# Kernel tuning notes

Hardware: AMD Instinct MI355X
Metric: run time of the kernel (lower is better)

The kernel has to match this reference:

```python
import jax, jax.numpy as jnp
import numpy as np

N = 50000      # nodes
E = 800000     # edges (avg degree 16)
G = 50         # graphs in batch (1000 nodes each)
D_IN, H, H2, OUT = 8, 128, 64, 1


def setup_inputs() -> dict:
    key = jax.random.key(0)
    ks = jax.random.split(key, 16)
    src = jax.random.randint(ks[0], (E,), 0, N)
    # every node gets at least one in-edge (forward computes 3/in_deg)
    dst = jnp.concatenate([jnp.arange(N), jax.random.randint(ks[1], (E - N,), 0, N)])
    graph_ids = jnp.arange(N) // (N // G)

    def lin(k, fan_in, fan_out):
        return jax.random.normal(k, (fan_in, fan_out), jnp.float32) / np.float32(np.sqrt(fan_in))

    inp = {"src": src, "dst": dst, "graph_ids": graph_ids}
    dims = [(D_IN, H), (H, H), (H, H), (H, H), (H, H)]
    for i, (fi, fo) in enumerate(dims):
        inp[f"W{i+1}"] = lin(ks[2 + i], fi, fo)
        inp[f"b{i+1}"] = jnp.zeros((fo,), jnp.float32)
    inp["lw1"] = lin(ks[8], H, H2)
    inp["lb1"] = jnp.zeros((H2,), jnp.float32)
    inp["lw2"] = lin(ks[9], H2, OUT)
    inp["lb2"] = jnp.zeros((OUT,), jnp.float32)
    return inp


def reference(src, dst, graph_ids, W1, b1, W2, b2, W3, b3, W4, b4, W5, b5, lw1, lb1, lw2, lb2):
    ones_e = jnp.ones((E,), jnp.float32)
    in_deg = jax.ops.segment_sum(ones_e, dst, num_segments=N)   # [N]
    out_deg = jax.ops.segment_sum(ones_e, src, num_segments=N)  # [N]

    # degree features (8 channels)
    h1 = in_deg[:, None]
    h2 = (in_deg > 3.0).astype(jnp.float32)[:, None]
    h3 = 3.0 / h1
    h4 = (in_deg > 4.0).astype(jnp.float32)[:, None]
    h_ = jnp.concatenate([h1, h2, h3, h4, -h1, -h2, -h3, -h4], axis=1)  # [N,8]

    # DGL GraphConv norm='both': clamp degrees to min 1 for normalization
    norm_src = jnp.maximum(out_deg, 1.0) ** -0.5  # [N]
    norm_dst = jnp.maximum(in_deg, 1.0) ** -0.5   # [N]

    def conv(h, W, b):
        m = (h * norm_src[:, None])[src]                        # [E, d] gather
        agg = jax.ops.segment_sum(m, dst, num_segments=N)       # [N, d] scatter-add
        return agg * norm_dst[:, None] @ W + b

    h_co = jax.nn.relu(conv(h_, W1, b1))
    h_co = jax.nn.relu(conv(h_co, W2, b2))
    h_co = jax.nn.relu(conv(h_co, W3, b3))
    h_co = jax.nn.relu(conv(h_co, W4, b4))
    h_co = jax.nn.relu(conv(h_co, W5, b5))                      # [N, H]

    # dgl.mean_nodes: per-graph mean pool
    counts = jax.ops.segment_sum(jnp.ones((N,), jnp.float32), graph_ids, num_segments=G)
    graph_emb = jax.ops.segment_sum(h_co, graph_ids, num_segments=G) / counts[:, None]  # [G, H]

    # dropout layers are identity in eval mode
    h_emb = jax.nn.relu(graph_emb @ lw1 + lb1)
    pred = jax.nn.sigmoid(h_emb @ lw2 + lb2)                    # [G, 1]
    return (pred, graph_emb, h_co)
```

## Files before the change

kernel.cpp:

```cpp
#include <hip/hip_runtime.h>
#include <math.h>

#define N_NODES 50000
#define N_EDGES 800000
#define N_GRAPHS 50
#define HD 128
#define TM 64
#define POOL_CHUNK 125
#define SCAN_B 256
#define SCAN_NB ((N_NODES + SCAN_B - 1) / SCAN_B)
#define NB_H 128
#define CH_H (N_EDGES / NB_H)
#define NBIN2 (N_NODES / 2)
#define ALDA 129

__global__ __launch_bounds__(256) void k_hist(const int* __restrict__ src,
                                              const int* __restrict__ dst,
                                              unsigned* __restrict__ part_in,
                                              unsigned* __restrict__ part_out) {
    __shared__ unsigned cnt[NBIN2];
    int t = threadIdx.x, b = blockIdx.x;
    int e0 = b * CH_H;
    for (int j = t; j < NBIN2; j += 256) cnt[j] = 0;
    __syncthreads();
    for (int e = e0 + t; e < e0 + CH_H; e += 256) {
        int i = dst[e];
        atomicAdd(&cnt[i >> 1], 1u << ((i & 1) * 16));
    }
    __syncthreads();
    for (int j = t; j < NBIN2; j += 256) part_in[b * NBIN2 + j] = cnt[j];
    __syncthreads();
    for (int j = t; j < NBIN2; j += 256) cnt[j] = 0;
    __syncthreads();
    for (int e = e0 + t; e < e0 + CH_H; e += 256) {
        int i = src[e];
        atomicAdd(&cnt[i >> 1], 1u << ((i & 1) * 16));
    }
    __syncthreads();
    for (int j = t; j < NBIN2; j += 256) part_out[b * NBIN2 + j] = cnt[j];
}

__global__ void k_dreduce(unsigned* __restrict__ part_in,
                          const unsigned* __restrict__ part_out,
                          int* __restrict__ deg_in, int* __restrict__ deg_out) {
    int j = blockIdx.x * blockDim.x + threadIdx.x;
    if (j >= NBIN2) return;
    unsigned run_i = 0, run_o = 0;
    for (int b = 0; b < NB_H; ++b) {
        unsigned pi = part_in[b * NBIN2 + j];
        unsigned po = part_out[b * NBIN2 + j];
        part_in[b * NBIN2 + j] = run_i;
        run_i += pi;
        run_o += po;
    }
    ((int2*)deg_in)[j] = make_int2((int)(run_i & 0xFFFFu), (int)(run_i >> 16));
    ((int2*)deg_out)[j] = make_int2((int)(run_o & 0xFFFFu), (int)(run_o >> 16));
}

__global__ void k_norms(const int* __restrict__ deg_in, const int* __restrict__ deg_out,
                        const int* __restrict__ gids,
                        float* norm_src, float* norm_dst, int* gcount,
                        float4* __restrict__ feat4) {
    __shared__ int hist[N_GRAPHS];
    int t = threadIdx.x;
    if (t < N_GRAPHS) hist[t] = 0;
    __syncthreads();
    int i = blockIdx.x * blockDim.x + t;
    if (i < N_NODES) {
        float di = (float)deg_in[i];
        float dq = (float)deg_out[i];
        float nd = 1.0f / sqrtf(fmaxf(di, 1.0f));
        float ns = 1.0f / sqrtf(fmaxf(dq, 1.0f));
        norm_dst[i] = nd;
        norm_src[i] = ns;
        float4 f;
        f.x = di * ns;
        f.y = (di > 3.0f) ? ns : 0.0f;
        f.z = (3.0f / di) * ns;
        f.w = (di > 4.0f) ? ns : 0.0f;
        feat4[i] = f;
        atomicAdd(&hist[gids[i]], 1);
    }
    __syncthreads();
    if (t < N_GRAPHS && hist[t] != 0) atomicAdd(&gcount[t], hist[t]);
}

__global__ void k_scan1(const int* __restrict__ deg_in, int* off, int* bsum) {
    __shared__ int sh[SCAN_B];
    int t = threadIdx.x;
    int i = blockIdx.x * SCAN_B + t;
    int v = (i < N_NODES) ? deg_in[i] : 0;
    sh[t] = v;
    __syncthreads();
    for (int o = 1; o < SCAN_B; o <<= 1) {
        int u = (t >= o) ? sh[t - o] : 0;
        __syncthreads();
        sh[t] += u;
        __syncthreads();
    }
    if (i < N_NODES) off[i] = sh[t] - v;
    if (t == SCAN_B - 1) bsum[blockIdx.x] = sh[t];
}

__global__ void k_scan2(int* bsum, int* off) {
    __shared__ int sh[SCAN_B];
    int t = threadIdx.x;
    int v = (t < SCAN_NB) ? bsum[t] : 0;
    sh[t] = v;
    __syncthreads();
    for (int o = 1; o < SCAN_B; o <<= 1) {
        int u = (t >= o) ? sh[t - o] : 0;
        __syncthreads();
        sh[t] += u;
        __syncthreads();
    }
    if (t < SCAN_NB) bsum[t] = sh[t] - v;
    if (t == SCAN_B - 1) off[N_NODES] = sh[t];
}

__global__ void k_scan3(int* off, const int* __restrict__ bsum) {
    int b = blockIdx.x, t = threadIdx.x;
    int i = b * SCAN_B + t;
    if (i < N_NODES) off[i] += bsum[b];
}

__global__ __launch_bounds__(256) void k_scatter2(const int* __restrict__ src,
                                                  const int* __restrict__ dst,
                                                  const int* __restrict__ off,
                                                  const unsigned* __restrict__ part_in,
                                                  int* __restrict__ csr) {
    __shared__ unsigned cur[NBIN2];
    int t = threadIdx.x, b = blockIdx.x;
    const unsigned* base = part_in + (size_t)b * NBIN2;
    for (int j = t; j < NBIN2; j += 256) cur[j] = base[j];
    __syncthreads();
    int e0 = b * CH_H;
    for (int e = e0 + t; e < e0 + CH_H; e += 256) {
        int d = dst[e];
        int sh = (d & 1) * 16;
        unsigned old = atomicAdd(&cur[d >> 1], 1u << sh);
        int rank = (int)((old >> sh) & 0xFFFFu);
        csr[off[d] + rank] = src[e];
    }
}

__global__ void k_agg1(const int* __restrict__ off, const int* __restrict__ csr,
                       const float4* __restrict__ feat4,
                       const float* __restrict__ ndst, float* __restrict__ agg8) {
    int i = blockIdx.x * blockDim.x + threadIdx.x;
    if (i >= N_NODES) return;
    int e0 = off[i], e1 = off[i + 1];
    float a0 = 0.f, a1 = 0.f, a2 = 0.f, a3 = 0.f;
    int e = e0;
    for (; e + 1 < e1; e += 2) {
        float4 f0 = feat4[csr[e]];
        float4 f1 = feat4[csr[e + 1]];
        a0 += f0.x + f1.x; a1 += f0.y + f1.y;
        a2 += f0.z + f1.z; a3 += f0.w + f1.w;
    }
    if (e < e1) {
        float4 f0 = feat4[csr[e]];
        a0 += f0.x; a1 += f0.y; a2 += f0.z; a3 += f0.w;
    }
    float nd = ndst[i];
    a0 *= nd; a1 *= nd; a2 *= nd; a3 *= nd;
    float4* p = (float4*)(agg8 + (size_t)i * 8);
    float4 hi = { a0, a1, a2, a3 };
    float4 lo = { -a0, -a1, -a2, -a3 };
    p[0] = hi;
    p[1] = lo;
}

__global__ void k_gemm1(const float* __restrict__ agg8, const float* __restrict__ W,
                        const float* __restrict__ b, const float* __restrict__ nsrc,
                        float* __restrict__ out) {
    __shared__ float Wsh[8 * 128];
    int t = threadIdx.x;
    for (int i = t; i < 1024; i += 256) Wsh[i] = W[i];
    __syncthreads();
    int row = blockIdx.x * 2 + (t >> 7);
    int j = t & 127;
    if (row >= N_NODES) return;
    const float* a = agg8 + (size_t)row * 8;
    float acc = b[j];
#pragma unroll
    for (int k = 0; k < 8; ++k) acc += a[k] * Wsh[k * 128 + j];
    out[(size_t)row * HD + j] = fmaxf(acc, 0.0f) * nsrc[row];
}

__global__ __launch_bounds__(256) void k_agg4(const int* __restrict__ off,
                                              const int* __restrict__ csr,
                                              const float* __restrict__ ndst,
                                              const float* __restrict__ h,
                                              float* __restrict__ out) {
    int wid = (blockIdx.x * blockDim.x + threadIdx.x) >> 6;
    int lane = threadIdx.x & 63;
    if (wid >= N_NODES) return;
    int half = lane >> 5;
    int q = lane & 31;
    int e0 = off[wid], e1 = off[wid + 1];
    float4 a = { 0.f, 0.f, 0.f, 0.f };
    int e = e0 + half;
    for (; e + 6 < e1; e += 8) {
        int s0 = csr[e], s1 = csr[e + 2], s2 = csr[e + 4], s3 = csr[e + 6];
        float4 v0 = *(const float4*)(h + (size_t)s0 * HD + q * 4);
        float4 v1 = *(const float4*)(h + (size_t)s1 * HD + q * 4);
        float4 v2 = *(const float4*)(h + (size_t)s2 * HD + q * 4);
        float4 v3 = *(const float4*)(h + (size_t)s3 * HD + q * 4);
        a.x += v0.x + v1.x + v2.x + v3.x;
        a.y += v0.y + v1.y + v2.y + v3.y;
        a.z += v0.z + v1.z + v2.z + v3.z;
        a.w += v0.w + v1.w + v2.w + v3.w;
    }
    for (; e < e1; e += 2) {
        int s0 = csr[e];
        float4 v0 = *(const float4*)(h + (size_t)s0 * HD + q * 4);
        a.x += v0.x; a.y += v0.y; a.z += v0.z; a.w += v0.w;
    }
    a.x += __shfl_xor(a.x, 32);
    a.y += __shfl_xor(a.y, 32);
    a.z += __shfl_xor(a.z, 32);
    a.w += __shfl_xor(a.w, 32);
    if (half == 0) {
        float nd = ndst[wid];
        a.x *= nd; a.y *= nd; a.z *= nd; a.w *= nd;
        *(float4*)(out + (size_t)wid * HD + q * 4) = a;
    }
}

__global__ void k_agg2(const int* __restrict__ off, const int* __restrict__ csr,
                       const float* __restrict__ ndst,
                       const float* __restrict__ h, float* __restrict__ out) {
    int wid = (blockIdx.x * blockDim.x + threadIdx.x) >> 6;
    int lane = threadIdx.x & 63;
    if (wid >= N_NODES) return;
    int e0 = off[wid], e1 = off[wid + 1];
    float a0 = 0.f, a1 = 0.f;
    int e = e0;
    for (; e + 3 < e1; e += 4) {
        int s0 = csr[e], s1 = csr[e + 1], s2 = csr[e + 2], s3 = csr[e + 3];
        float2 v0 = *(const float2*)(h + (size_t)s0 * HD + lane * 2);
        float2 v1 = *(const float2*)(h + (size_t)s1 * HD + lane * 2);
        float2 v2 = *(const float2*)(h + (size_t)s2 * HD + lane * 2);
        float2 v3 = *(const float2*)(h + (size_t)s3 * HD + lane * 2);
        a0 += v0.x + v1.x + v2.x + v3.x;
        a1 += v0.y + v1.y + v2.y + v3.y;
    }
    for (; e < e1; ++e) {
        int s0 = csr[e];
        float2 v0 = *(const float2*)(h + (size_t)s0 * HD + lane * 2);
        a0 += v0.x; a1 += v0.y;
    }
    float nd = ndst[wid];
    float2 o; o.x = a0 * nd; o.y = a1 * nd;
    *(float2*)(out + (size_t)wid * HD + lane * 2) = o;
}

__global__ __launch_bounds__(256) void k_gemm2(const float* __restrict__ A,
                                               const float* __restrict__ W,
                                               const float* __restrict__ b,
                                               const float* __restrict__ nsrc,
                                               int premult,
                                               float* __restrict__ out) {
    __shared__ float Wsh[128 * 64];
    __shared__ float Ash[64 * ALDA];
    int t = threadIdx.x;
    int row0 = blockIdx.x * TM;
    int jh = blockIdx.y * 64;
    const float4* W4 = (const float4*)W;
#pragma unroll
    for (int i = 0; i < 8; ++i) {
        int idx = t + i * 256;
        int k = idx >> 4;
        int q = idx & 15;
        ((float4*)Wsh)[k * 16 + q] = W4[k * 32 + (jh >> 2) + q];
    }
    const float4* A4 = (const float4*)A;
#pragma unroll
    for (int i = 0; i < 8; ++i) {
        int idx = t + i * 256;
        int r = idx >> 5;
        int q = idx & 31;
        int row = row0 + r;
        if (row >= N_NODES) row = N_NODES - 1;
        float4 v = A4[(size_t)row * 32 + q];
        float* ap = &Ash[r * ALDA + 4 * q];
        ap[0] = v.x; ap[1] = v.y; ap[2] = v.z; ap[3] = v.w;
    }
    __syncthreads();
    int jq = (t & 15) * 4;
    int r0 = (t >> 4) * 4;
    float4 bv = *(const float4*)(b + jh + jq);
    float acc[4][4];
#pragma unroll
    for (int r = 0; r < 4; ++r) {
        acc[r][0] = bv.x; acc[r][1] = bv.y; acc[r][2] = bv.z; acc[r][3] = bv.w;
    }
#pragma unroll 4
    for (int k = 0; k < 128; ++k) {
        float4 wv = *(const float4*)&Wsh[k * 64 + jq];
        float a0 = Ash[(r0 + 0) * ALDA + k];
        float a1 = Ash[(r0 + 1) * ALDA + k];
        float a2 = Ash[(r0 + 2) * ALDA + k];
        float a3 = Ash[(r0 + 3) * ALDA + k];
        acc[0][0] += a0 * wv.x; acc[0][1] += a0 * wv.y; acc[0][2] += a0 * wv.z; acc[0][3] += a0 * wv.w;
        acc[1][0] += a1 * wv.x; acc[1][1] += a1 * wv.y; acc[1][2] += a1 * wv.z; acc[1][3] += a1 * wv.w;
        acc[2][0] += a2 * wv.x; acc[2][1] += a2 * wv.y; acc[2][2] += a2 * wv.z; acc[2][3] += a2 * wv.w;
        acc[3][0] += a3 * wv.x; acc[3][1] += a3 * wv.y; acc[3][2] += a3 * wv.z; acc[3][3] += a3 * wv.w;
    }
#pragma unroll
    for (int r = 0; r < 4; ++r) {
        int row = row0 + r0 + r;
        if (row < N_NODES) {
            float sc = premult ? nsrc[row] : 1.0f;
            float* op = out + (size_t)row * HD + jh + jq;
            float2 o01 = { fmaxf(acc[r][0], 0.f) * sc, fmaxf(acc[r][1], 0.f) * sc };
            float2 o23 = { fmaxf(acc[r][2], 0.f) * sc, fmaxf(acc[r][3], 0.f) * sc };
            *(float2*)op = o01;
            *(float2*)(op + 2) = o23;
        }
    }
}

__global__ void k_pool(const float* __restrict__ hco, const int* __restrict__ gids,
                       float* gsum) {
    int f = threadIdx.x;
    int n0 = blockIdx.x * POOL_CHUNK;
    int g = gids[n0];
    float s = 0.f;
    for (int i = 0; i < POOL_CHUNK; ++i)
        s += hco[(size_t)(n0 + i) * HD + f];
    atomicAdd(&gsum[g * HD + f], s);
}

__global__ void k_head(const float* __restrict__ gsum, const int* __restrict__ gcount,
                       const float* __restrict__ lw1, const float* __restrict__ lb1,
                       const float* __restrict__ lw2, const float* __restrict__ lb2,
                       float* __restrict__ dout) {
    __shared__ float ge[128];
    int g = blockIdx.x, j = threadIdx.x;
    float cnt = (float)gcount[g];
    float g0 = gsum[g * HD + j] / cnt;
    float g1 = gsum[g * HD + 64 + j] / cnt;
    ge[j] = g0; ge[64 + j] = g1;
    dout[N_GRAPHS + g * HD + j] = g0;
    dout[N_GRAPHS + g * HD + 64 + j] = g1;
    __syncthreads();
    float acc = lb1[j];
#pragma unroll 4
    for (int k = 0; k < 128; ++k) acc += ge[k] * lw1[k * 64 + j];
    float he = fmaxf(acc, 0.f);
    float p = he * lw2[j];
#pragma unroll
    for (int o = 32; o > 0; o >>= 1) p += __shfl_down(p, o);
    if (j == 0) dout[g] = 1.0f / (1.0f + expf(-(p + lb2[0])));
}

extern "C" void kernel_launch(void* const* d_in, const int* in_sizes, int n_in,
                              void* d_out, int out_size, void* d_ws, size_t ws_size,
                              hipStream_t stream) {
    const int* src  = (const int*)d_in[0];
    const int* dst  = (const int*)d_in[1];
    const int* gids = (const int*)d_in[2];
    const float* W1 = (const float*)d_in[3];  const float* b1 = (const float*)d_in[4];
    const float* W2 = (const float*)d_in[5];  const float* b2 = (const float*)d_in[6];
    const float* W3 = (const float*)d_in[7];  const float* b3 = (const float*)d_in[8];
    const float* W4 = (const float*)d_in[9];  const float* b4 = (const float*)d_in[10];
    const float* W5 = (const float*)d_in[11]; const float* b5 = (const float*)d_in[12];
    const float* lw1 = (const float*)d_in[13]; const float* lb1 = (const float*)d_in[14];
    const float* lw2 = (const float*)d_in[15]; const float* lb2 = (const float*)d_in[16];
    float* out = (float*)d_out;

    char* ws = (char*)d_ws;
    int*    gcount   = (int*)(ws + 0);
    float*  gsum     = (float*)(ws + 256);
    const size_t ZERO_BYTES = 25856;
    int*    deg_in   = (int*)(ws + 26112);
    int*    deg_out  = (int*)(ws + 226304);
    int*    off      = (int*)(ws + 426496);
    int*    csr      = (int*)(ws + 826880);
    float*  norm_src = (float*)(ws + 4026880);
    float*  norm_dst = (float*)(ws + 4227072);
    int*    bsum     = (int*)(ws + 4427264);
    float4* feat4    = (float4*)(ws + 4428288);
    float*  aggbuf   = (float*)(ws + 5228544);
    float*  hws      = (float*)(ws + 30828544);
    const size_t WS_NEEDED = 30828544 + 25600000;

    unsigned* part_in  = (unsigned*)aggbuf;
    unsigned* part_out = (unsigned*)aggbuf + NB_H * NBIN2;

    float* hco = out + (N_GRAPHS + N_GRAPHS * HD);
    bool aligned = (ws_size >= WS_NEEDED);
    float* hbuf = aligned ? hws : hco;

    hipMemsetAsync(ws, 0, ZERO_BYTES, stream);

    k_hist<<<NB_H, 256, 0, stream>>>(src, dst, part_in, part_out);
    k_dreduce<<<(NBIN2 + 255) / 256, 256, 0, stream>>>(part_in, part_out,
                                                       deg_in, deg_out);
    k_norms<<<(N_NODES + 255) / 256, 256, 0, stream>>>(deg_in, deg_out, gids,
                                                       norm_src, norm_dst, gcount, feat4);
    k_scan1<<<SCAN_NB, SCAN_B, 0, stream>>>(deg_in, off, bsum);
    k_scan2<<<1, SCAN_B, 0, stream>>>(bsum, off);
    k_scan3<<<SCAN_NB, SCAN_B, 0, stream>>>(off, bsum);
    k_scatter2<<<NB_H, 256, 0, stream>>>(src, dst, off, part_in, csr);

    k_agg1<<<(N_NODES + 255) / 256, 256, 0, stream>>>(off, csr, feat4, norm_dst, aggbuf);
    k_gemm1<<<N_NODES / 2, 256, 0, stream>>>(aggbuf, W1, b1, norm_src, hbuf);

    const float* Ws[4] = { W2, W3, W4, W5 };
    const float* bs[4] = { b2, b3, b4, b5 };
    dim3 ggrid((N_NODES + TM - 1) / TM, 2);
    for (int L = 0; L < 4; ++L) {
        if (aligned)
            k_agg4<<<(N_NODES * 64 + 255) / 256, 256, 0, stream>>>(off, csr,
                                                                   norm_dst, hbuf, aggbuf);
        else
            k_agg2<<<(N_NODES * 64 + 255) / 256, 256, 0, stream>>>(off, csr,
                                                                   norm_dst, hbuf, aggbuf);
        float* gout = (L < 3) ? hbuf : hco;
        k_gemm2<<<ggrid, 256, 0, stream>>>(aggbuf, Ws[L], bs[L],
                                           norm_src, (L < 3) ? 1 : 0, gout);
    }

    k_pool<<<N_NODES / POOL_CHUNK, 128, 0, stream>>>(hco, gids, gsum);
    k_head<<<N_GRAPHS, 64, 0, stream>>>(gsum, gcount, lw1, lb1, lw2, lb2, out);
}
```

Baseline: 487.3 us.

## Store hidden features in column strips and aggregate one strip per pass

Hidden features are now written in a strip-blocked layout of 16-column strips, each covering all nodes (strip-major). The aggregation kernel gets eight passes, each gathering one 16-float strip per neighbour, so the working set per pass (about 3.2 MB) can stay in cache instead of scattering across the full 25.6 MB feature matrix. The GEMM kernels gain a layout flag to write this blocked format, and CSR index loads and aggregate stores become nontemporal. The cost is that the CSR index array is re-read eight times, and gathers use narrower 64-byte segments.

```diff
diff --git a/kernel.cpp b/kernel.cpp
--- a/kernel.cpp
+++ b/kernel.cpp
@@ -13,6 +13,8 @@
 #define CH_H (N_EDGES / NB_H)
 #define NBIN2 (N_NODES / 2)
 #define ALDA 129
+#define NPASS 8
+#define STRIP 16
 
 __global__ __launch_bounds__(256) void k_hist(const int* __restrict__ src,
                                               const int* __restrict__ dst,
@@ -173,7 +175,7 @@
 
 __global__ void k_gemm1(const float* __restrict__ agg8, const float* __restrict__ W,
                         const float* __restrict__ b, const float* __restrict__ nsrc,
-                        float* __restrict__ out) {
+                        int blocked, float* __restrict__ out) {
     __shared__ float Wsh[8 * 128];
     int t = threadIdx.x;
     for (int i = t; i < 1024; i += 256) Wsh[i] = W[i];
@@ -185,46 +187,49 @@
     float acc = b[j];
 #pragma unroll
     for (int k = 0; k < 8; ++k) acc += a[k] * Wsh[k * 128 + j];
-    out[(size_t)row * HD + j] = fmaxf(acc, 0.0f) * nsrc[row];
-}
-
-__global__ __launch_bounds__(256) void k_agg4(const int* __restrict__ off,
+    float v = fmaxf(acc, 0.0f) * nsrc[row];
+    if (blocked)
+        out[((size_t)(j >> 4) * N_NODES + row) * STRIP + (j & 15)] = v;
+    else
+        out[(size_t)row * HD + j] = v;
+}
+
+__global__ __launch_bounds__(256) void k_aggx(const int* __restrict__ off,
                                               const int* __restrict__ csr,
                                               const float* __restrict__ ndst,
                                               const float* __restrict__ h,
-                                              float* __restrict__ out) {
-    int wid = (blockIdx.x * blockDim.x + threadIdx.x) >> 6;
+                                              float* __restrict__ agg) {
+    int bx = blockIdx.x;
+    int pass = bx & 7;
+    int node = (bx >> 3) * 4 + (threadIdx.x >> 6);
     int lane = threadIdx.x & 63;
-    if (wid >= N_NODES) return;
-    int half = lane >> 5;
-    int q = lane & 31;
-    int e0 = off[wid], e1 = off[wid + 1];
-    float4 a = { 0.f, 0.f, 0.f, 0.f };
-    int e = e0 + half;
-    for (; e + 6 < e1; e += 8) {
-        int s0 = csr[e], s1 = csr[e + 2], s2 = csr[e + 4], s3 = csr[e + 6];
-        float4 v0 = *(const float4*)(h + (size_t)s0 * HD + q * 4);
-        float4 v1 = *(const float4*)(h + (size_t)s1 * HD + q * 4);
-        float4 v2 = *(const float4*)(h + (size_t)s2 * HD + q * 4);
-        float4 v3 = *(const float4*)(h + (size_t)s3 * HD + q * 4);
-        a.x += v0.x + v1.x + v2.x + v3.x;
-        a.y += v0.y + v1.y + v2.y + v3.y;
-        a.z += v0.z + v1.z + v2.z + v3.z;
-        a.w += v0.w + v1.w + v2.w + v3.w;
-    }
-    for (; e < e1; e += 2) {
-        int s0 = csr[e];
-        float4 v0 = *(const float4*)(h + (size_t)s0 * HD + q * 4);
-        a.x += v0.x; a.y += v0.y; a.z += v0.z; a.w += v0.w;
-    }
-    a.x += __shfl_xor(a.x, 32);
-    a.y += __shfl_xor(a.y, 32);
-    a.z += __shfl_xor(a.z, 32);
-    a.w += __shfl_xor(a.w, 32);
-    if (half == 0) {
-        float nd = ndst[wid];
-        a.x *= nd; a.y *= nd; a.z *= nd; a.w *= nd;
-        *(float4*)(out + (size_t)wid * HD + q * 4) = a;
+    int slot = lane >> 3, q = lane & 7;
+    const float* hp = h + (size_t)pass * (N_NODES * STRIP);
+    int e0 = off[node], e1 = off[node + 1];
+    float a0 = 0.f, a1 = 0.f;
+    int e = e0 + slot;
+    for (; e + 8 < e1; e += 16) {
+        int s0 = __builtin_nontemporal_load(csr + e);
+        int s1 = __builtin_nontemporal_load(csr + e + 8);
+        float2 v0 = *(const float2*)(hp + (size_t)s0 * STRIP + q * 2);
+        float2 v1 = *(const float2*)(hp + (size_t)s1 * STRIP + q * 2);
+        a0 += v0.x + v1.x;
+        a1 += v0.y + v1.y;
+    }
+    for (; e < e1; e += 8) {
+        int s0 = __builtin_nontemporal_load(csr + e);
+        float2 v0 = *(const float2*)(hp + (size_t)s0 * STRIP + q * 2);
+        a0 += v0.x;
+        a1 += v0.y;
+    }
+    a0 += __shfl_xor(a0, 8);  a1 += __shfl_xor(a1, 8);
+    a0 += __shfl_xor(a0, 16); a1 += __shfl_xor(a1, 16);
+    a0 += __shfl_xor(a0, 32); a1 += __shfl_xor(a1, 32);
+    if (slot == 0) {
+        float nd = ndst[node];
+        float* op = agg + (size_t)node * HD + pass * STRIP + q * 2;
+        __builtin_nontemporal_store(a0 * nd, op);
+        __builtin_nontemporal_store(a1 * nd, op + 1);
     }
 }
 
@@ -260,7 +265,7 @@
                                                const float* __restrict__ W,
                                                const float* __restrict__ b,
                                                const float* __restrict__ nsrc,
-                                               int premult,
+                                               int premult, int blocked,
                                                float* __restrict__ out) {
     __shared__ float Wsh[128 * 64];
     __shared__ float Ash[64 * ALDA];
@@ -308,12 +313,19 @@
         acc[2][0] += a2 * wv.x; acc[2][1] += a2 * wv.y; acc[2][2] += a2 * wv.z; acc[2][3] += a2 * wv.w;
         acc[3][0] += a3 * wv.x; acc[3][1] += a3 * wv.y; acc[3][2] += a3 * wv.z; acc[3][3] += a3 * wv.w;
     }
+    int j = jh + jq;
 #pragma unroll
     for (int r = 0; r < 4; ++r) {
         int row = row0 + r0 + r;
-        if (row < N_NODES) {
-            float sc = premult ? nsrc[row] : 1.0f;
-            float* op = out + (size_t)row * HD + jh + jq;
+        if (row >= N_NODES) continue;
+        float sc = premult ? nsrc[row] : 1.0f;
+        if (blocked) {
+            float* op = out + ((size_t)(j >> 4) * N_NODES + row) * STRIP + (j & 15);
+            float4 o = { fmaxf(acc[r][0], 0.f) * sc, fmaxf(acc[r][1], 0.f) * sc,
+                         fmaxf(acc[r][2], 0.f) * sc, fmaxf(acc[r][3], 0.f) * sc };
+            *(float4*)op = o;
+        } else {
+            float* op = out + (size_t)row * HD + j;
             float2 o01 = { fmaxf(acc[r][0], 0.f) * sc, fmaxf(acc[r][1], 0.f) * sc };
             float2 o23 = { fmaxf(acc[r][2], 0.f) * sc, fmaxf(acc[r][3], 0.f) * sc };
             *(float2*)op = o01;
@@ -392,7 +404,6 @@
 
     float* hco = out + (N_GRAPHS + N_GRAPHS * HD);
     bool aligned = (ws_size >= WS_NEEDED);
-    float* hbuf = aligned ? hws : hco;
 
     hipMemsetAsync(ws, 0, ZERO_BYTES, stream);
 
@@ -407,21 +418,27 @@
     k_scatter2<<<NB_H, 256, 0, stream>>>(src, dst, off, part_in, csr);
 
     k_agg1<<<(N_NODES + 255) / 256, 256, 0, stream>>>(off, csr, feat4, norm_dst, aggbuf);
-    k_gemm1<<<N_NODES / 2, 256, 0, stream>>>(aggbuf, W1, b1, norm_src, hbuf);
+    float* hbuf = aligned ? hws : hco;
+    k_gemm1<<<N_NODES / 2, 256, 0, stream>>>(aggbuf, W1, b1, norm_src,
+                                             aligned ? 1 : 0, hbuf);
 
     const float* Ws[4] = { W2, W3, W4, W5 };
     const float* bs[4] = { b2, b3, b4, b5 };
     dim3 ggrid((N_NODES + TM - 1) / TM, 2);
     for (int L = 0; L < 4; ++L) {
-        if (aligned)
-            k_agg4<<<(N_NODES * 64 + 255) / 256, 256, 0, stream>>>(off, csr,
-                                                                   norm_dst, hbuf, aggbuf);
-        else
+        int premult = (L < 3) ? 1 : 0;
+        if (aligned) {
+            k_aggx<<<(N_NODES / 4) * NPASS, 256, 0, stream>>>(off, csr, norm_dst,
+                                                              hws, aggbuf);
+            float* gout = (L < 3) ? hws : hco;
+            k_gemm2<<<ggrid, 256, 0, stream>>>(aggbuf, Ws[L], bs[L], norm_src,
+                                               premult, (L < 3) ? 1 : 0, gout);
+        } else {
             k_agg2<<<(N_NODES * 64 + 255) / 256, 256, 0, stream>>>(off, csr,
-                                                                   norm_dst, hbuf, aggbuf);
-        float* gout = (L < 3) ? hbuf : hco;
-        k_gemm2<<<ggrid, 256, 0, stream>>>(aggbuf, Ws[L], bs[L],
-                                           norm_src, (L < 3) ? 1 : 0, gout);
+                                                                   norm_dst, hco, aggbuf);
+            k_gemm2<<<ggrid, 256, 0, stream>>>(aggbuf, Ws[L], bs[L], norm_src,
+                                               premult, 0, hco);
+        }
     }
 
     k_pool<<<N_NODES / POOL_CHUNK, 128, 0, stream>>>(hco, gids, gsum);
```

New measurement: 826.2 us. +69.6%, slower.
